# Kernel tuning notes

Hardware: AMD Instinct MI355X
Metric: run time of the kernel (lower is better)

The kernel has to match this reference:

```python
import jax, jax.numpy as jnp
import numpy as np


def setup_inputs() -> dict:
    key = jax.random.key(0)
    k0, k1, k2, k3, k4 = jax.random.split(key, 5)
    B, W, C, C2, D = 4, 64, 512, 512, 64  # D = C // k, k=8
    x = jax.random.normal(k0, (B, W, W, C), dtype=jnp.float32)
    input_h = jax.random.normal(k1, (B, W, W, C2), dtype=jnp.float32)
    f = jax.random.normal(k2, (1, 1, C2, D), dtype=jnp.float32) * 0.02
    g = jax.random.normal(k3, (1, 1, C, D), dtype=jnp.float32) * 0.02
    gamma = jax.random.uniform(k4, (1,), dtype=jnp.float32)
    return {"x": x, "input_h": input_h, "f": f, "g": g, "gamma": gamma}


def reference(x, input_h, f, g, gamma):
    # x: [B,W,W,C] NHWC, input_h: [B,W,W,C2], f: [1,1,C2,D], g: [1,1,C,D]
    B, W, _, C = x.shape
    C2 = input_h.shape[-1]
    N = W * W
    # 1x1 convs == per-pixel channel matmuls
    f_proj = jnp.einsum('bhwc,cd->bhwd', input_h, f[0, 0])  # [B,W,W,D]
    g_proj = jnp.einsum('bhwc,cd->bhwd', x, g[0, 0])        # [B,W,W,D]
    f_flat = f_proj.reshape(B, N, -1)
    g_flat = g_proj.reshape(B, N, -1)
    # unscaled attention scores over spatial positions
    s = jnp.einsum('bnd,bmd->bnm', g_flat, f_flat)          # [B,N,N]
    beta = jax.nn.softmax(s, axis=-1)
    h_flat = input_h.reshape(B, N, C2)
    o = jnp.einsum('bnm,bmc->bnc', beta, h_flat).reshape(B, W, W, C2)
    # mix_concat == 'mix': learned residual mix
    return gamma * o + x
```

## Files before the change

kernel.cpp:

```cpp
#include <hip/hip_runtime.h>
#include <hip/hip_bf16.h>
#include <cstdint>
#include <cstddef>


#define NPOS 4096
#define CCH  512
#define DQK  64
#define LSTR 72

typedef __attribute__((ext_vector_type(8)))  short s8v;
typedef __attribute__((ext_vector_type(4)))  short s4v;
typedef __attribute__((ext_vector_type(4)))  float f4v;

__device__ __forceinline__ float bf2f(unsigned short u) {
    unsigned int x = ((unsigned int)u) << 16;
    return __builtin_bit_cast(float, x);
}
__device__ __forceinline__ unsigned short f2bf(float f) {
    unsigned int u = __builtin_bit_cast(unsigned int, f);
    u += 0x7fffu + ((u >> 16) & 1u);
    return (unsigned short)(u >> 16);
}

__global__ __launch_bounds__(256) void wt_kernel(
    const float* __restrict__ f, const float* __restrict__ g,
    unsigned short* __restrict__ fT, unsigned short* __restrict__ gT)
{
    int gid = blockIdx.x * 256 + threadIdx.x;
    for (int e = 0; e < 4; ++e) {
        int i = e * 16384 + gid;
        int which = i >> 15;
        int j = i & 32767;
        int d = j >> 9, k = j & 511;
        const float* s = which ? g : f;
        unsigned short* dst = which ? gT : fT;
        dst[j] = f2bf(s[k * 64 + d]);
    }
}

__global__ __launch_bounds__(256) void vt_kernel(
    const float* __restrict__ ih, unsigned short* __restrict__ Vt)
{
    __shared__ unsigned short T[64 * 65];
    const int tid = threadIdx.x;
    const int bidx = blockIdx.x;
    const int bb = bidx >> 9;
    const int rem = bidx & 511;
    const int ct = rem >> 6;
    const int nt = rem & 63;

    for (int p = 0; p < 4; ++p) {
        int idx = p * 256 + tid;
        int r = idx >> 4, gg = idx & 15;
        f4v v = *(const f4v*)(ih + ((size_t)bb * NPOS + nt * 64 + r) * CCH + ct * 64 + gg * 4);
        for (int j = 0; j < 4; ++j) T[r * 65 + gg * 4 + j] = f2bf(v[j]);
    }
    __syncthreads();
    for (int p = 0; p < 2; ++p) {
        int idx = p * 256 + tid;
        int c = idx >> 3, ng = idx & 7;
        unsigned short tmp[8];
        for (int j = 0; j < 8; ++j) tmp[j] = T[(ng * 8 + j) * 65 + c];
        *(s8v*)(Vt + ((size_t)bb * CCH + ct * 64 + c) * NPOS + nt * 64 + ng * 8) = *(const s8v*)tmp;
    }
}

__global__ __launch_bounds__(256) void proj_kernel(
    const float* __restrict__ x,  const float* __restrict__ ih,
    const unsigned short* __restrict__ gT, const unsigned short* __restrict__ fT,
    unsigned short* __restrict__ Qg, unsigned short* __restrict__ Kf)
{
    __shared__ __align__(16) short Alds[128 * LSTR];
    __shared__ __align__(16) short Wlds[64 * LSTR];
    const int tid = threadIdx.x;
    const int wave = tid >> 6, lane = tid & 63;
    const int n15 = lane & 15, quad = lane >> 4;
    const int which = blockIdx.x >> 7;
    const int rb = (blockIdx.x & 127) * 128;
    const float* src = which ? ih : x;
    const unsigned short* wT  = which ? fT : gT;
    unsigned short* dst = which ? Kf : Qg;

    f4v acc[2][4];
    for (int i = 0; i < 2; ++i)
        for (int j = 0; j < 4; ++j)
            acc[i][j] = f4v{0.f, 0.f, 0.f, 0.f};

    for (int kc = 0; kc < 8; ++kc) {
        for (int p = 0; p < 8; ++p) {
            int idx = p * 256 + tid;
            int r = idx >> 4, gg = idx & 15;
            f4v v = *(const f4v*)(src + (size_t)(rb + r) * CCH + kc * 64 + gg * 4);
            s4v tv;
            for (int j = 0; j < 4; ++j) tv[j] = (short)f2bf(v[j]);
            *(s4v*)&Alds[r * LSTR + gg * 4] = tv;
        }
        for (int p = 0; p < 2; ++p) {
            int idx = p * 256 + tid;
            int c = idx >> 3, gg = idx & 7;
            *(s8v*)&Wlds[c * LSTR + gg * 8] =
                *(const s8v*)(wT + (size_t)c * CCH + kc * 64 + gg * 8);
        }
        __syncthreads();
        for (int kk = 0; kk < 2; ++kk) {
            s8v af0 = *(const s8v*)&Alds[(wave * 32 +      n15) * LSTR + kk * 32 + quad * 8];
            s8v af1 = *(const s8v*)&Alds[(wave * 32 + 16 + n15) * LSTR + kk * 32 + quad * 8];
            for (int ct = 0; ct < 4; ++ct) {
                s8v bf = *(const s8v*)&Wlds[(ct * 16 + n15) * LSTR + kk * 32 + quad * 8];
                acc[0][ct] = __builtin_amdgcn_mfma_f32_16x16x32_bf16(af0, bf, acc[0][ct], 0, 0, 0);
                acc[1][ct] = __builtin_amdgcn_mfma_f32_16x16x32_bf16(af1, bf, acc[1][ct], 0, 0, 0);
            }
        }
        __syncthreads();
    }
    for (int rt = 0; rt < 2; ++rt)
        for (int ct = 0; ct < 4; ++ct)
            for (int r = 0; r < 4; ++r) {
                int row = wave * 32 + rt * 16 + quad * 4 + r;
                int col = ct * 16 + n15;
                dst[(size_t)(rb + row) * DQK + col] = f2bf(acc[rt][ct][r]);
            }
}

__global__ __launch_bounds__(1024) void flash_kernel(
    const unsigned short* __restrict__ Qg,
    const unsigned short* __restrict__ Kf,
    const unsigned short* __restrict__ Vt,
    const float* __restrict__ xin,
    const float* __restrict__ gptr,
    float* __restrict__ out)
{
    __shared__ __align__(16) short Klds[2 * 64 * LSTR];
    __shared__ __align__(16) short Plds[2 * 64 * LSTR];
    __shared__ float l_part[4][64];
    __shared__ float l_s[64];

    const int tid = threadIdx.x;
    const int wave = tid >> 6;
    const int lane = tid & 63;
    const int n15 = lane & 15, quad = lane >> 4;
    const int bid = blockIdx.x;
    const int xcd = bid & 7;
    const int b = xcd >> 1;
    const int qt = (xcd & 1) + ((bid >> 3) << 1);
    const int qbase = qt * 64;

    const float SOFT_M = 20.0f;

    f4v acc[4][2];
    for (int i = 0; i < 4; ++i)
        for (int j = 0; j < 2; ++j)
            acc[i][j] = f4v{0.f, 0.f, 0.f, 0.f};
    f4v lsum = f4v{0.f, 0.f, 0.f, 0.f};

    const int ti = wave >> 2;
    const int mi = wave & 3;
    s8v qf[2];
    {
        const unsigned short* qp =
            Qg + ((size_t)b * NPOS + qbase + ti * 16 + n15) * DQK + quad * 8;
        qf[0] = *(const s8v*)(qp);
        qf[1] = *(const s8v*)(qp + 32);
    }

    const int cb = wave * 32;
    const unsigned short* vp0 =
        Vt + ((size_t)b * CCH + cb + n15) * NPOS + quad * 8;
    const unsigned short* vp1 = vp0 + (size_t)16 * NPOS;

    const int kr = tid >> 3, kg = tid & 7;
    const unsigned short* kbase_p = Kf + ((size_t)b * NPOS + kr) * DQK + kg * 8;
    s8v kreg;
    if (tid < 512) {
        kreg = *(const s8v*)(kbase_p);
        *(s8v*)&Klds[kr * LSTR + kg * 8] = kreg;
        kreg = *(const s8v*)(kbase_p + (size_t)64 * DQK);
    }
    __syncthreads();

    for (int kb = 0; kb < NPOS / 64; ++kb) {
        const int m0 = kb * 64;
        s8v vf[2][2];
        vf[0][0] = *(const s8v*)(vp0 + m0);
        vf[0][1] = *(const s8v*)(vp0 + m0 + 32);
        vf[1][0] = *(const s8v*)(vp1 + m0);
        vf[1][1] = *(const s8v*)(vp1 + m0 + 32);
        if (tid < 512 && kb + 1 < NPOS / 64) {
            *(s8v*)&Klds[((kb + 1) & 1) * 64 * LSTR + kr * LSTR + kg * 8] = kreg;
            if (kb + 2 < NPOS / 64)
                kreg = *(const s8v*)(kbase_p + (size_t)(m0 + 128) * DQK);
        }

        {
            const short* Kb = &Klds[(kb & 1) * 64 * LSTR];
            short* Pb = &Plds[(kb & 1) * 64 * LSTR];
            f4v s4 = f4v{0.f, 0.f, 0.f, 0.f};
            s8v kf0 = *(const s8v*)&Kb[(mi * 16 + n15) * LSTR + quad * 8];
            s8v kf1 = *(const s8v*)&Kb[(mi * 16 + n15) * LSTR + 32 + quad * 8];
            s4 = __builtin_amdgcn_mfma_f32_16x16x32_bf16(qf[0], kf0, s4, 0, 0, 0);
            s4 = __builtin_amdgcn_mfma_f32_16x16x32_bf16(qf[1], kf1, s4, 0, 0, 0);
            const int col = mi * 16 + n15;
            const int row0 = ti * 16 + quad * 4;
            for (int r = 0; r < 4; ++r) {
                unsigned short pb = f2bf(__expf(fminf(s4[r], 80.0f) - SOFT_M));
                Pb[(row0 + r) * LSTR + col] = (short)pb;
                lsum[r] += bf2f(pb);
            }
        }
        __syncthreads();

        {
            const short* Pb = &Plds[(kb & 1) * 64 * LSTR];
            for (int kk = 0; kk < 2; ++kk) {
                for (int q4 = 0; q4 < 4; ++q4) {
                    s8v af = *(const s8v*)&Pb[(q4 * 16 + n15) * LSTR + kk * 32 + quad * 8];
                    acc[q4][0] = __builtin_amdgcn_mfma_f32_16x16x32_bf16(
                        af, vf[0][kk], acc[q4][0], 0, 0, 0);
                    acc[q4][1] = __builtin_amdgcn_mfma_f32_16x16x32_bf16(
                        af, vf[1][kk], acc[q4][1], 0, 0, 0);
                }
            }
        }
    }

    for (int d = 1; d < 16; d <<= 1)
        for (int r = 0; r < 4; ++r)
            lsum[r] += __shfl_xor(lsum[r], d);
    if (n15 == 0)
        for (int r = 0; r < 4; ++r)
            l_part[mi][ti * 16 + quad * 4 + r] = lsum[r];
    __syncthreads();
    if (tid < 64)
        l_s[tid] = l_part[0][tid] + l_part[1][tid] + l_part[2][tid] + l_part[3][tid];
    __syncthreads();

    const float gamma = gptr[0];
    for (int q4 = 0; q4 < 4; ++q4) {
        for (int r = 0; r < 4; ++r) {
            const int row = q4 * 16 + quad * 4 + r;
            const float sc = gamma / l_s[row];
            const size_t base = ((size_t)b * NPOS + qbase + row) * CCH;
            const int col0 = cb + n15;
            const int col1 = cb + 16 + n15;
            out[base + col0] = acc[q4][0][r] * sc + xin[base + col0];
            out[base + col1] = acc[q4][1][r] * sc + xin[base + col1];
        }
    }
}

extern "C" void kernel_launch(void* const* d_in, const int* in_sizes, int n_in,
                              void* d_out, int out_size, void* d_ws, size_t ws_size,
                              hipStream_t stream)
{
    const float* x     = (const float*)d_in[0];
    const float* ih    = (const float*)d_in[1];
    const float* f     = (const float*)d_in[2];
    const float* g     = (const float*)d_in[3];
    const float* gamma = (const float*)d_in[4];
    float* out = (float*)d_out;

    char* ws = (char*)d_ws;
    unsigned short* fT = (unsigned short*)(ws + 0);
    unsigned short* gT = (unsigned short*)(ws + 65536);
    unsigned short* Qg = (unsigned short*)(ws + 131072);
    unsigned short* Kf = (unsigned short*)(ws + 2228224);
    unsigned short* Vt = (unsigned short*)(ws + 4325376);

    wt_kernel<<<64, 256, 0, stream>>>(f, g, fT, gT);
    vt_kernel<<<2048, 256, 0, stream>>>(ih, Vt);
    proj_kernel<<<256, 256, 0, stream>>>(x, ih, gT, fT, Qg, Kf);
    flash_kernel<<<256, 1024, 0, stream>>>(Qg, Kf, Vt, x, gamma, out);
}
```

Baseline: 276.6 us.

## Prefetch next tiles into registers and use LDS-only barriers

The projection kernel now loads the next K-chunk of activations and weights into registers while the current chunk is computed, so global loads no longer sit on the critical path. The flash kernel prefetches the next V fragments one iteration ahead, double-buffering them in registers. __syncthreads is replaced by a barrier that waits only on LDS counters (lgkmcnt), so outstanding global loads are not drained at each barrier. This raises register pressure and relies on the custom barrier being a sufficient memory fence.

Measured after the change: 247.0 us. -10.7%, faster.

```diff
diff --git a/kernel.cpp b/kernel.cpp
--- a/kernel.cpp
+++ b/kernel.cpp
@@ -21,6 +21,11 @@
     unsigned int u = __builtin_bit_cast(unsigned int, f);
     u += 0x7fffu + ((u >> 16) & 1u);
     return (unsigned short)(u >> 16);
+}
+
+__device__ __forceinline__ void sync_lds() {
+    asm volatile("s_waitcnt lgkmcnt(0)" ::: "memory");
+    __builtin_amdgcn_s_barrier();
 }
 
 __global__ __launch_bounds__(256) void wt_kernel(
@@ -87,22 +92,47 @@
         for (int j = 0; j < 4; ++j)
             acc[i][j] = f4v{0.f, 0.f, 0.f, 0.f};
 
+    const int ar = tid >> 4, ag = tid & 15;
+    f4v areg[8];
+    s8v wreg[2];
+    for (int p = 0; p < 8; ++p) {
+        int idx = p * 256 + tid;
+        int r = idx >> 4, gg = idx & 15;
+        areg[p] = *(const f4v*)(src + (size_t)(rb + r) * CCH + gg * 4);
+    }
+    for (int p = 0; p < 2; ++p) {
+        int idx = p * 256 + tid;
+        int c = idx >> 3, gg = idx & 7;
+        wreg[p] = *(const s8v*)(wT + (size_t)c * CCH + gg * 8);
+    }
+    (void)ar; (void)ag;
+
     for (int kc = 0; kc < 8; ++kc) {
         for (int p = 0; p < 8; ++p) {
             int idx = p * 256 + tid;
             int r = idx >> 4, gg = idx & 15;
-            f4v v = *(const f4v*)(src + (size_t)(rb + r) * CCH + kc * 64 + gg * 4);
             s4v tv;
-            for (int j = 0; j < 4; ++j) tv[j] = (short)f2bf(v[j]);
+            for (int j = 0; j < 4; ++j) tv[j] = (short)f2bf(areg[p][j]);
             *(s4v*)&Alds[r * LSTR + gg * 4] = tv;
         }
         for (int p = 0; p < 2; ++p) {
             int idx = p * 256 + tid;
             int c = idx >> 3, gg = idx & 7;
-            *(s8v*)&Wlds[c * LSTR + gg * 8] =
-                *(const s8v*)(wT + (size_t)c * CCH + kc * 64 + gg * 8);
-        }
-        __syncthreads();
+            *(s8v*)&Wlds[c * LSTR + gg * 8] = wreg[p];
+        }
+        if (kc < 7) {
+            for (int p = 0; p < 8; ++p) {
+                int idx = p * 256 + tid;
+                int r = idx >> 4, gg = idx & 15;
+                areg[p] = *(const f4v*)(src + (size_t)(rb + r) * CCH + (kc + 1) * 64 + gg * 4);
+            }
+            for (int p = 0; p < 2; ++p) {
+                int idx = p * 256 + tid;
+                int c = idx >> 3, gg = idx & 7;
+                wreg[p] = *(const s8v*)(wT + (size_t)c * CCH + (kc + 1) * 64 + gg * 8);
+            }
+        }
+        sync_lds();
         for (int kk = 0; kk < 2; ++kk) {
             s8v af0 = *(const s8v*)&Alds[(wave * 32 +      n15) * LSTR + kk * 32 + quad * 8];
             s8v af1 = *(const s8v*)&Alds[(wave * 32 + 16 + n15) * LSTR + kk * 32 + quad * 8];
@@ -112,7 +142,7 @@
                 acc[1][ct] = __builtin_amdgcn_mfma_f32_16x16x32_bf16(af1, bf, acc[1][ct], 0, 0, 0);
             }
         }
-        __syncthreads();
+        sync_lds();
     }
     for (int rt = 0; rt < 2; ++rt)
         for (int ct = 0; ct < 4; ++ct)
@@ -177,15 +207,21 @@
         *(s8v*)&Klds[kr * LSTR + kg * 8] = kreg;
         kreg = *(const s8v*)(kbase_p + (size_t)64 * DQK);
     }
-    __syncthreads();
+    s8v vfc[2][2];
+    vfc[0][0] = *(const s8v*)(vp0);
+    vfc[0][1] = *(const s8v*)(vp0 + 32);
+    vfc[1][0] = *(const s8v*)(vp1);
+    vfc[1][1] = *(const s8v*)(vp1 + 32);
+    sync_lds();
 
     for (int kb = 0; kb < NPOS / 64; ++kb) {
         const int m0 = kb * 64;
-        s8v vf[2][2];
-        vf[0][0] = *(const s8v*)(vp0 + m0);
-        vf[0][1] = *(const s8v*)(vp0 + m0 + 32);
-        vf[1][0] = *(const s8v*)(vp1 + m0);
-        vf[1][1] = *(const s8v*)(vp1 + m0 + 32);
+        const int mn = (kb + 1 < NPOS / 64) ? m0 + 64 : m0;
+        s8v vfn[2][2];
+        vfn[0][0] = *(const s8v*)(vp0 + mn);
+        vfn[0][1] = *(const s8v*)(vp0 + mn + 32);
+        vfn[1][0] = *(const s8v*)(vp1 + mn);
+        vfn[1][1] = *(const s8v*)(vp1 + mn + 32);
         if (tid < 512 && kb + 1 < NPOS / 64) {
             *(s8v*)&Klds[((kb + 1) & 1) * 64 * LSTR + kr * LSTR + kg * 8] = kreg;
             if (kb + 2 < NPOS / 64)
@@ -208,7 +244,7 @@
                 lsum[r] += bf2f(pb);
             }
         }
-        __syncthreads();
+        sync_lds();
 
         {
             const short* Pb = &Plds[(kb & 1) * 64 * LSTR];
@@ -216,12 +252,14 @@
                 for (int q4 = 0; q4 < 4; ++q4) {
                     s8v af = *(const s8v*)&Pb[(q4 * 16 + n15) * LSTR + kk * 32 + quad * 8];
                     acc[q4][0] = __builtin_amdgcn_mfma_f32_16x16x32_bf16(
-                        af, vf[0][kk], acc[q4][0], 0, 0, 0);
+                        af, vfc[0][kk], acc[q4][0], 0, 0, 0);
                     acc[q4][1] = __builtin_amdgcn_mfma_f32_16x16x32_bf16(
-                        af, vf[1][kk], acc[q4][1], 0, 0, 0);
+                        af, vfc[1][kk], acc[q4][1], 0, 0, 0);
                 }
             }
         }
+        vfc[0][0] = vfn[0][0]; vfc[0][1] = vfn[0][1];
+        vfc[1][0] = vfn[1][0]; vfc[1][1] = vfn[1][1];
     }
 
     for (int d = 1; d < 16; d <<= 1)
```
